# Kernel optimization log

Measured on AMD Instinct MI355X. Metric: run time of the kernel, lower is better.

## Reference

```python
import jax, jax.numpy as jnp
import numpy as np

N = 50000      # total nodes in batched graph
E = 800000     # total edges (avg degree 16)
B = 512        # number of graphs in batch
F_IN = 74      # input node feature size
H = 64         # hidden size per layer
OUT = 64       # output_feats
EPS = 1e-5     # BatchNorm eps


def setup_inputs() -> dict:
    key = jax.random.key(0)
    ks = jax.random.split(key, 32)
    d = {}
    d['feats'] = jax.random.normal(ks[0], (N, F_IN), dtype=jnp.float32)
    d['src'] = jax.random.randint(ks[1], (E,), 0, N)
    d['dst'] = jax.random.randint(ks[2], (E,), 0, N)
    d['graph_ids'] = jnp.sort(jax.random.randint(ks[3], (N,), 0, B))
    dims = [F_IN, H, H, H]
    i = 4
    for l in range(3):
        din, dout = dims[l], dims[l + 1]
        d[f'W{l}'] = jax.random.normal(ks[i], (din, dout), jnp.float32) / np.sqrt(din).astype(np.float32); i += 1
        d[f'b{l}'] = jnp.zeros((dout,), jnp.float32)
        d[f'rW{l}'] = jax.random.normal(ks[i], (din, dout), jnp.float32) / np.sqrt(din).astype(np.float32); i += 1
        d[f'rb{l}'] = jnp.zeros((dout,), jnp.float32)
        d[f'g{l}'] = jnp.ones((dout,), jnp.float32)    # BN gamma
        d[f'be{l}'] = jnp.zeros((dout,), jnp.float32)  # BN beta
    d['aw_W'] = jax.random.normal(ks[i], (H, 1), jnp.float32) / np.sqrt(H).astype(np.float32); i += 1
    d['aw_b'] = jnp.zeros((1,), jnp.float32)
    d['out_W'] = jax.random.normal(ks[i], (2 * H, OUT), jnp.float32) / np.sqrt(2 * H).astype(np.float32); i += 1
    d['out_b'] = jnp.zeros((OUT,), jnp.float32)
    return d


def _gcn_layer(x, src, dst, W, b, rW, rb, g, be):
    # GraphConv, norm='none': out = sum-aggregate(X W) + b, then relu
    xw = x @ W                                                    # [N, dout]
    agg = jax.ops.segment_sum(xw[src], dst, num_segments=N) + b   # gather/scatter over edges
    h = jax.nn.relu(agg)
    # residual: relu(Linear(x))
    h = h + jax.nn.relu(x @ rW + rb)
    # dropout p=0 -> identity
    # BatchNorm1d (training-mode batch statistics, biased variance)
    mean = jnp.mean(h, axis=0)
    var = jnp.var(h, axis=0)
    return (h - mean) * jax.lax.rsqrt(var + EPS) * g + be


def reference(feats, src, dst, graph_ids,
              W0, b0, rW0, rb0, g0, be0,
              W1, b1, rW1, rb1, g1, be1,
              W2, b2, rW2, rb2, g2, be2,
              aw_W, aw_b, out_W, out_b):
    h = feats
    h = _gcn_layer(h, src, dst, W0, b0, rW0, rb0, g0, be0)
    h = _gcn_layer(h, src, dst, W1, b1, rW1, rb1, g1, be1)
    h = _gcn_layer(h, src, dst, W2, b2, rW2, rb2, g2, be2)
    # WeightedSumAndMax readout
    w = jax.nn.sigmoid(h @ aw_W + aw_b)                               # [N, 1]
    h_sum = jax.ops.segment_sum(h * w, graph_ids, num_segments=B)     # [B, H]
    h_max = jax.ops.segment_max(h, graph_ids, num_segments=B)         # [B, H]
    h_max = jnp.where(jnp.isfinite(h_max), h_max, 0.0)                # empty graphs -> 0 (dgl max_nodes)
    h_g = jnp.concatenate([h_sum, h_max], axis=1)                     # [B, 2H]
    return h_g @ out_W + out_b                                        # [B, OUT]
```

## Files before the change

### kernel.cpp

```cpp
#include <hip/hip_runtime.h>
#include <hip/hip_bf16.h>
#include <math.h>

#define NN 50000
#define NE 800000
#define NB 512
#define FIN 74
#define HD 64
#define BN_EPS 1e-5f

#define CHUNK 32
#define ELLW 32
#define NBLK ((NN + CHUNK - 1) / CHUNK)
#define NBUCK2 NBLK
#define EB2 128
#define EPB (NE / EB2)
#define OCAPW 96


__global__ __launch_bounds__(256) void hist2_kernel(const int* __restrict__ dst,
                                                    int* __restrict__ H,
                                                    float* __restrict__ stats012,
                                                    unsigned long long* __restrict__ xw_zrow,
                                                    const float* __restrict__ W0,
                                                    const float* __restrict__ rW0,
                                                    float2* __restrict__ Wpk0) {
    __shared__ int lh[NBUCK2];
    int b = blockIdx.x, tid = threadIdx.x;
    for (int i = tid; i < NBUCK2; i += 256) lh[i] = 0;
    __syncthreads();
    int e0 = b * EPB;
    for (int i = tid; i < EPB; i += 256) atomicAdd(&lh[dst[e0 + i] >> 5], 1);
    if (b == 0) {
        for (int i = tid; i < 384; i += 256) stats012[i] = 0.f;
        if (tid < 16) xw_zrow[tid] = 0ull;
        for (int i = tid; i < FIN * HD; i += 256) Wpk0[i] = make_float2(W0[i], rW0[i]);
    }
    __syncthreads();
    for (int i = tid; i < NBUCK2; i += 256) H[b * NBUCK2 + i] = lh[i];
}

__global__ __launch_bounds__(128) void scanA2_kernel(int* __restrict__ H, int* __restrict__ T) {
    __shared__ int l[128];
    int k = blockIdx.x, tid = threadIdx.x;
    int v = H[tid * NBUCK2 + k];
    l[tid] = v;
    __syncthreads();
    for (int off = 1; off < 128; off <<= 1) {
        int t = (tid >= off) ? l[tid - off] : 0;
        __syncthreads();
        l[tid] += t;
        __syncthreads();
    }
    H[tid * NBUCK2 + k] = l[tid] - v;
    if (tid == 127) T[k] = l[127];
}

__global__ __launch_bounds__(256) void scanB2_kernel(const int* __restrict__ T,
                                                     int* __restrict__ bbase) {
    __shared__ int l[256];
    __shared__ int carry;
    int tid = threadIdx.x;
    if (tid == 0) carry = 0;
    __syncthreads();
    for (int c0 = 0; c0 < NBUCK2; c0 += 256) {
        int v = (c0 + tid < NBUCK2) ? T[c0 + tid] : 0;
        l[tid] = v;
        __syncthreads();
        for (int off = 1; off < 256; off <<= 1) {
            int t = (tid >= off) ? l[tid - off] : 0;
            __syncthreads();
            l[tid] += t;
            __syncthreads();
        }
        if (c0 + tid < NBUCK2) bbase[c0 + tid] = l[tid] - v + carry;
        __syncthreads();
        if (tid == 0) carry += l[255];
        __syncthreads();
    }
    if (tid == 0) bbase[NBUCK2] = carry;
}

__global__ __launch_bounds__(256) void scatter2_kernel(const int* __restrict__ src,
                                                       const int* __restrict__ dst,
                                                       const int* __restrict__ H,
                                                       const int* __restrict__ bbase,
                                                       unsigned* __restrict__ pairs) {
    __shared__ int cur[NBUCK2];
    int b = blockIdx.x, tid = threadIdx.x;
    for (int i = tid; i < NBUCK2; i += 256) cur[i] = H[b * NBUCK2 + i] + bbase[i];
    __syncthreads();
    int e0 = b * EPB;
    for (int i = tid; i < EPB; i += 256) {
        int d = dst[e0 + i];
        int s = src[e0 + i];
        int pos = atomicAdd(&cur[d >> 5], 1);
        pairs[pos] = (unsigned)s | ((unsigned)(d & 31) << 17);
    }
}


template <int K>
__global__ __launch_bounds__(256) void gemm_dual_kernel(
    const float* __restrict__ x, const float2* __restrict__ Wpk,
    const float* __restrict__ rb, __hip_bfloat16* __restrict__ xw,
    __hip_bfloat16* __restrict__ res, int n) {
    __shared__ float2 sW[K * HD];
    __shared__ float srb[64];
    for (int i = threadIdx.x; i < K * HD; i += 256) sW[i] = Wpk[i];
    if (threadIdx.x < 64) srb[threadIdx.x] = rb[threadIdx.x];
    __syncthreads();
    int wl = threadIdx.x >> 6, lane = threadIdx.x & 63;
    for (int r0 = (blockIdx.x * 4 + wl) * 8; r0 < n; r0 += gridDim.x * 32) {
        float a1[8], a2[8];
#pragma unroll
        for (int r = 0; r < 8; ++r) { a1[r] = 0.f; a2[r] = 0.f; }
#pragma unroll
        for (int c0 = 0; c0 < K; c0 += 64) {
            const int cl = (K - c0 < 64) ? (K - c0) : 64;
            float xv[8];
#pragma unroll
            for (int r = 0; r < 8; ++r) {
                int row = r0 + r;
                xv[r] = (lane < cl && row < n) ? x[(size_t)row * K + c0 + lane] : 0.f;
            }
#pragma unroll 16
            for (int j = 0; j < cl; ++j) {
                float2 w = sW[(c0 + j) * HD + lane];
#pragma unroll
                for (int r = 0; r < 8; ++r) {
                    float xb = __uint_as_float(
                        __builtin_amdgcn_readlane(__float_as_uint(xv[r]), j));
                    a1[r] = fmaf(xb, w.x, a1[r]);
                    a2[r] = fmaf(xb, w.y, a2[r]);
                }
            }
        }
#pragma unroll
        for (int r = 0; r < 8; ++r) {
            int row = r0 + r;
            if (row < n) {
                xw[(size_t)row * HD + lane] = __float2bfloat16(a1[r]);
                res[(size_t)row * HD + lane] = __float2bfloat16(fmaxf(a2[r] + srb[lane], 0.f));
            }
        }
    }
}

__global__ void fold_kernel(const float* __restrict__ stats, const float* __restrict__ g,
                            const float* __restrict__ be, const float* __restrict__ W,
                            const float* __restrict__ rW, const float* __restrict__ rb,
                            float2* __restrict__ Wpk, float* __restrict__ shiftW,
                            float* __restrict__ rbp) {
    __shared__ float sc[64], sh[64];
    int t = threadIdx.x;
    if (t < 64) {
        float mean = stats[t] / (float)NN;
        float var = stats[64 + t] / (float)NN - mean * mean;
        float scale = g[t] * rsqrtf(var + BN_EPS);
        sc[t] = scale;
        sh[t] = be[t] - mean * scale;
    }
    __syncthreads();
    for (int i = t; i < 64 * 64; i += 256) {
        int k = i >> 6;
        Wpk[i] = make_float2(sc[k] * W[i], sc[k] * rW[i]);
    }
    if (t < 64) {
        float sw = 0.f, srw = 0.f;
        for (int k = 0; k < 64; ++k) {
            sw = fmaf(sh[k], W[k * 64 + t], sw);
            srw = fmaf(sh[k], rW[k * 64 + t], srw);
        }
        shiftW[t] = sw;
        rbp[t] = rb[t] + srw;
    }
}

__device__ __forceinline__ float bf_lo(unsigned int p) { return __uint_as_float(p << 16); }
__device__ __forceinline__ float bf_hi(unsigned int p) { return __uint_as_float(p & 0xffff0000u); }

#define GATHER16(BASE)                                             \
    {                                                              \
        unsigned long long d[16];                                  \
        _Pragma("unroll") for (int j = 0; j < 16; ++j) {           \
            int idx = myIdx[(BASE) + j];                           \
            unsigned off = (unsigned)idx * 16u + (unsigned)c8;     \
            d[j] = XWu[off];                                       \
        }                                                          \
        _Pragma("unroll") for (int j = 0; j < 16; ++j) {           \
            unsigned lo = (unsigned)d[j], hi = (unsigned)(d[j] >> 32); \
            a0 += bf_lo(lo); a1 += bf_hi(lo);                      \
            a2 += bf_lo(hi); a3 += bf_hi(hi);                      \
        }                                                          \
    }

__global__ __launch_bounds__(256, 6) void fused_agg_kernel(
    const __hip_bfloat16* __restrict__ xw, const __hip_bfloat16* __restrict__ res,
    const float* __restrict__ b, const float* __restrict__ shiftW,
    const int* __restrict__ bbase, const unsigned* __restrict__ pairs,
    float* __restrict__ hout, float* __restrict__ stats, int n) {
    __shared__ int sIdx[4][8][ELLW + 1];
    __shared__ int sLen[4][8];
    __shared__ unsigned oflow[4][OCAPW];
    __shared__ int ocnt[4];
    __shared__ float lsr[4][16][8];

    int tid = threadIdx.x;
    int wl = tid >> 6, lane = tid & 63;
    int r0 = blockIdx.x * CHUNK;

    for (int i = lane; i < 8 * (ELLW + 1); i += 64) ((int*)sIdx[wl])[i] = NN;
    if (lane < 8) sLen[wl][lane] = 0;
    if (lane == 0) ocnt[wl] = 0;

    int beg = bbase[blockIdx.x], end = bbase[blockIdx.x + 1];
    for (int i = beg + lane; i < end; i += 64) {
        unsigned v = pairs[i];
        int rloc = (int)(v >> 17);
        if ((rloc >> 3) == wl) {
            int r8 = rloc & 7;
            int rk = atomicAdd(&sLen[wl][r8], 1);
            if (rk < ELLW) {
                sIdx[wl][r8][rk] = (int)(v & 0x1FFFFu);
            } else {
                int o = atomicAdd(&ocnt[wl], 1);
                if (o < OCAPW) oflow[wl][o] = v;
            }
        }
    }
    int nof = ocnt[wl];
    int noflow = (nof < OCAPW) ? nof : OCAPW;

    const unsigned long long* XWu = (const unsigned long long*)xw;
    const unsigned long long* REu = (const unsigned long long*)res;
    int q = lane >> 4, c8 = lane & 15;
    float4 bv = *(const float4*)&b[4 * c8];
    float4 swv = shiftW ? *(const float4*)&shiftW[4 * c8] : make_float4(0.f, 0.f, 0.f, 0.f);
    float s0 = 0.f, s1 = 0.f, s2 = 0.f, s3 = 0.f;
    float q0 = 0.f, q1 = 0.f, q2 = 0.f, q3 = 0.f;

#pragma unroll
    for (int p = 0; p < 2; ++p) {
        int r8 = p * 4 + q;
        int grow = r0 + wl * 8 + r8;
        int growc = (grow < n) ? grow : (n - 1);
        int l0 = sLen[wl][p * 4], l1 = sLen[wl][p * 4 + 1];
        int l2 = sLen[wl][p * 4 + 2], l3 = sLen[wl][p * 4 + 3];
        int m01 = (l0 > l1) ? l0 : l1, m23 = (l2 > l3) ? l2 : l3;
        int kmax = (m01 > m23) ? m01 : m23;
        int mylen = sLen[wl][r8];
        const int* myIdx = sIdx[wl][r8];
        unsigned long long rqw = REu[(unsigned)growc * 16u + (unsigned)c8];
        float a0 = 0.f, a1 = 0.f, a2 = 0.f, a3 = 0.f;
        GATHER16(0)
        if (kmax > 16) GATHER16(16)
        if (kmax > ELLW) {
            int myrloc = wl * 8 + r8;
            for (int o = 0; o < noflow; ++o) {
                unsigned v = oflow[wl][o];
                if ((int)(v >> 17) == myrloc) {
                    unsigned off = (v & 0x1FFFFu) * 16u + (unsigned)c8;
                    unsigned long long u = XWu[off];
                    unsigned lo = (unsigned)u, hi = (unsigned)(u >> 32);
                    a0 += bf_lo(lo); a1 += bf_hi(lo);
                    a2 += bf_lo(hi); a3 += bf_hi(hi);
                }
            }
        }
        unsigned rlo = (unsigned)rqw, rhi = (unsigned)(rqw >> 32);
        float dg = (float)mylen;
        float h0 = fmaxf(a0 + fmaf(dg, swv.x, bv.x), 0.f) + bf_lo(rlo);
        float h1 = fmaxf(a1 + fmaf(dg, swv.y, bv.y), 0.f) + bf_hi(rlo);
        float h2 = fmaxf(a2 + fmaf(dg, swv.z, bv.z), 0.f) + bf_lo(rhi);
        float h3 = fmaxf(a3 + fmaf(dg, swv.w, bv.w), 0.f) + bf_hi(rhi);
        if (grow < n) {
            *(float4*)&hout[(unsigned)grow * 64u + 4u * c8] = make_float4(h0, h1, h2, h3);
            s0 += h0; s1 += h1; s2 += h2; s3 += h3;
            q0 += h0 * h0; q1 += h1 * h1; q2 += h2 * h2; q3 += h3 * h3;
        }
    }

    s0 += __shfl_xor(s0, 16, 64); s0 += __shfl_xor(s0, 32, 64);
    s1 += __shfl_xor(s1, 16, 64); s1 += __shfl_xor(s1, 32, 64);
    s2 += __shfl_xor(s2, 16, 64); s2 += __shfl_xor(s2, 32, 64);
    s3 += __shfl_xor(s3, 16, 64); s3 += __shfl_xor(s3, 32, 64);
    q0 += __shfl_xor(q0, 16, 64); q0 += __shfl_xor(q0, 32, 64);
    q1 += __shfl_xor(q1, 16, 64); q1 += __shfl_xor(q1, 32, 64);
    q2 += __shfl_xor(q2, 16, 64); q2 += __shfl_xor(q2, 32, 64);
    q3 += __shfl_xor(q3, 16, 64); q3 += __shfl_xor(q3, 32, 64);
    if (q == 0) {
        lsr[wl][c8][0] = s0; lsr[wl][c8][1] = s1; lsr[wl][c8][2] = s2; lsr[wl][c8][3] = s3;
        lsr[wl][c8][4] = q0; lsr[wl][c8][5] = q1; lsr[wl][c8][6] = q2; lsr[wl][c8][7] = q3;
    }
    __syncthreads();
    if (tid < 64) {
        int c8i = tid >> 2, comp = tid & 3;
        float ssum = lsr[0][c8i][comp] + lsr[1][c8i][comp] + lsr[2][c8i][comp] + lsr[3][c8i][comp];
        float qsum = lsr[0][c8i][4 + comp] + lsr[1][c8i][4 + comp] + lsr[2][c8i][4 + comp] +
                     lsr[3][c8i][4 + comp];
        atomicAdd(&stats[tid], ssum);
        atomicAdd(&stats[64 + tid], qsum);
    }
}


__global__ void readout_init_kernel(float* __restrict__ hsum, unsigned int* __restrict__ hmax,
                                    const float* __restrict__ stats, const float* __restrict__ g,
                                    const float* __restrict__ be, float* __restrict__ ss) {
    int idx = blockIdx.x * 256 + threadIdx.x;
    if (idx < NB * HD) {
        hsum[idx] = 0.f;
        hmax[idx] = 0x007FFFFFu;
    }
    if (blockIdx.x == 0 && threadIdx.x < 64) {
        int c = threadIdx.x;
        float mean = stats[c] / (float)NN;
        float var = stats[64 + c] / (float)NN - mean * mean;
        float scale = g[c] * rsqrtf(var + BN_EPS);
        ss[c] = scale;
        ss[64 + c] = be[c] - mean * scale;
    }
}

#define RNODES 16

__device__ __forceinline__ void ro_flush(float* hsum, unsigned int* hmax, int g, int c,
                                         float accS, float accM) {
    atomicAdd(&hsum[g * HD + c], accS);
    unsigned int bits = __float_as_uint(accM);
    unsigned int enc = (bits & 0x80000000u) ? ~bits : (bits | 0x80000000u);
    atomicMax(&hmax[g * HD + c], enc);
}

__global__ __launch_bounds__(256) void readout_kernel(
    const float* __restrict__ h, const int* __restrict__ gid, const float* __restrict__ ss,
    const float* __restrict__ awW, const float* __restrict__ awb, float* __restrict__ hsum,
    unsigned int* __restrict__ hmax, int n) {
    int wid = blockIdx.x * 4 + (threadIdx.x >> 6);
    int c = threadIdx.x & 63;
    int r0 = wid * RNODES;
    if (r0 >= n) return;
    int r1 = r0 + RNODES;
    if (r1 > n) r1 = n;
    float aw = awW[c], ab = awb[0];
    float sA = ss[c], sB = ss[64 + c];
    int cur = gid[r0];
    float accS = 0.f, accM = -__builtin_inff();
    for (int r = r0; r < r1; ++r) {
        int g = gid[r];
        if (g != cur) {
            ro_flush(hsum, hmax, cur, c, accS, accM);
            accS = 0.f;
            accM = -__builtin_inff();
            cur = g;
        }
        float v = fmaf(h[(size_t)r * HD + c], sA, sB);
        float p = v * aw;
        for (int off = 32; off; off >>= 1) p += __shfl_xor(p, off, 64);
        float w = 1.f / (1.f + expf(-(p + ab)));
        accS = fmaf(v, w, accS);
        accM = fmaxf(accM, v);
    }
    ro_flush(hsum, hmax, cur, c, accS, accM);
}

__global__ void final_kernel(const float* __restrict__ hsum, const unsigned int* __restrict__ hmax,
                             const float* __restrict__ outW, const float* __restrict__ outb,
                             float* __restrict__ out) {
    __shared__ float sW[128 * 64];
    for (int i = threadIdx.x; i < 128 * 64; i += 256) sW[i] = outW[i];
    __syncthreads();
    int idx = blockIdx.x * 256 + threadIdx.x;
    if (idx >= NB * HD) return;
    int bi = idx >> 6, o = idx & 63;
    float acc = outb[o];
#pragma unroll 4
    for (int k = 0; k < 64; ++k) acc = fmaf(hsum[bi * 64 + k], sW[k * 64 + o], acc);
#pragma unroll 4
    for (int k = 0; k < 64; ++k) {
        unsigned int e = hmax[bi * 64 + k];
        float m;
        if (e == 0x007FFFFFu) {
            m = 0.f;
        } else {
            m = (e & 0x80000000u) ? __uint_as_float(e ^ 0x80000000u) : __uint_as_float(~e);
        }
        acc = fmaf(m, sW[(64 + k) * 64 + o], acc);
    }
    out[idx] = acc;
}


extern "C" void kernel_launch(void* const* d_in, const int* in_sizes, int n_in,
                              void* d_out, int out_size, void* d_ws, size_t ws_size,
                              hipStream_t stream) {
    const float* feats = (const float*)d_in[0];
    const int* src = (const int*)d_in[1];
    const int* dst = (const int*)d_in[2];
    const int* gid = (const int*)d_in[3];
    const float* W[3];
    const float* b[3];
    const float* rW[3];
    const float* rb[3];
    const float* g[3];
    const float* be[3];
    for (int l = 0; l < 3; ++l) {
        W[l] = (const float*)d_in[4 + 6 * l + 0];
        b[l] = (const float*)d_in[4 + 6 * l + 1];
        rW[l] = (const float*)d_in[4 + 6 * l + 2];
        rb[l] = (const float*)d_in[4 + 6 * l + 3];
        g[l] = (const float*)d_in[4 + 6 * l + 4];
        be[l] = (const float*)d_in[4 + 6 * l + 5];
    }
    const float* awW = (const float*)d_in[22];
    const float* awb = (const float*)d_in[23];
    const float* outW = (const float*)d_in[24];
    const float* outb = (const float*)d_in[25];
    float* out = (float*)d_out;

    __hip_bfloat16* XW = (__hip_bfloat16*)d_ws;
    __hip_bfloat16* RES = XW + (size_t)(NN + 1) * HD;
    float* P1 = (float*)(RES + (size_t)NN * HD);
    float* stats = P1 + (size_t)NN * HD;
    float* ss2 = stats + 384;
    float2* WPK = (float2*)(ss2 + 128);
    float* shW = (float*)(WPK + FIN * HD);
    float* rbp = shW + 64;
    float* hsum = rbp + 64;
    unsigned int* hmax = (unsigned int*)(hsum + (size_t)NB * HD);
    unsigned* pairs = (unsigned*)(hmax + (size_t)NB * HD);
    int* H = (int*)(pairs + (size_t)NE);
    int* T = H + (size_t)EB2 * NBUCK2;
    int* bbase = T + NBUCK2;

    float* stats0 = stats;
    float* stats1 = stats + 128;
    float* stats2 = stats + 256;

    const int GEMMBLK = 1280;
    const int ROBLK = (NN + RNODES * 4 - 1) / (RNODES * 4);

    hist2_kernel<<<EB2, 256, 0, stream>>>(dst, H, stats,
                                          (unsigned long long*)(XW + (size_t)NN * HD),
                                          W[0], rW[0], WPK);
    scanA2_kernel<<<NBUCK2, 128, 0, stream>>>(H, T);
    scanB2_kernel<<<1, 256, 0, stream>>>(T, bbase);
    scatter2_kernel<<<EB2, 256, 0, stream>>>(src, dst, H, bbase, pairs);

    gemm_dual_kernel<FIN><<<GEMMBLK, 256, 0, stream>>>(feats, WPK, rb[0], XW, RES, NN);
    fused_agg_kernel<<<NBLK, 256, 0, stream>>>(XW, RES, b[0], (const float*)nullptr, bbase,
                                               pairs, P1, stats0, NN);

    fold_kernel<<<1, 256, 0, stream>>>(stats0, g[0], be[0], W[1], rW[1], rb[1], WPK, shW, rbp);
    gemm_dual_kernel<HD><<<GEMMBLK, 256, 0, stream>>>(P1, WPK, rbp, XW, RES, NN);
    fused_agg_kernel<<<NBLK, 256, 0, stream>>>(XW, RES, b[1], shW, bbase, pairs, P1, stats1, NN);

    fold_kernel<<<1, 256, 0, stream>>>(stats1, g[1], be[1], W[2], rW[2], rb[2], WPK, shW, rbp);
    gemm_dual_kernel<HD><<<GEMMBLK, 256, 0, stream>>>(P1, WPK, rbp, XW, RES, NN);
    fused_agg_kernel<<<NBLK, 256, 0, stream>>>(XW, RES, b[2], shW, bbase, pairs, P1, stats2, NN);

    readout_init_kernel<<<(NB * HD + 255) / 256, 256, 0, stream>>>(hsum, hmax, stats2, g[2], be[2], ss2);
    readout_kernel<<<ROBLK, 256, 0, stream>>>(P1, gid, ss2, awW, awb, hsum, hmax, NN);
    final_kernel<<<(NB * HD + 255) / 256, 256, 0, stream>>>(hsum, hmax, outW, outb, out);
}
```

Before: 322.2 us.

## Store packed GEMM weights as bf16 pairs and retune edge-bucket and GEMM grids

Packs the folded W and rW weights into one 32-bit word holding two bf16 values instead of a float2. This halves the shared-memory footprint and LDS traffic in the dual GEMM, at the cost of lower weight precision. It also doubles the number of edge-histogram blocks, with the scan block size following EB2, and lowers the GEMM grid from 1280 to 782 blocks. The smaller shared-memory allocation may let more GEMM blocks stay resident per CU. The bf16 weights add rounding error before each BatchNorm stage.

```diff
diff --git a/kernel.cpp b/kernel.cpp
--- a/kernel.cpp
+++ b/kernel.cpp
@@ -13,9 +13,15 @@
 #define ELLW 32
 #define NBLK ((NN + CHUNK - 1) / CHUNK)
 #define NBUCK2 NBLK
-#define EB2 128
+#define EB2 256
 #define EPB (NE / EB2)
 #define OCAPW 96
+
+__device__ __forceinline__ unsigned pack_bf2(float a, float b) {
+    __hip_bfloat16 ha = __float2bfloat16(a), hb = __float2bfloat16(b);
+    unsigned short ua = *(unsigned short*)&ha, ub = *(unsigned short*)&hb;
+    return (unsigned)ua | ((unsigned)ub << 16);
+}
 
 
 __global__ __launch_bounds__(256) void hist2_kernel(const int* __restrict__ dst,
@@ -24,7 +30,7 @@
                                                     unsigned long long* __restrict__ xw_zrow,
                                                     const float* __restrict__ W0,
                                                     const float* __restrict__ rW0,
-                                                    float2* __restrict__ Wpk0) {
+                                                    unsigned* __restrict__ Wpk0) {
     __shared__ int lh[NBUCK2];
     int b = blockIdx.x, tid = threadIdx.x;
     for (int i = tid; i < NBUCK2; i += 256) lh[i] = 0;
@@ -34,26 +40,26 @@
     if (b == 0) {
         for (int i = tid; i < 384; i += 256) stats012[i] = 0.f;
         if (tid < 16) xw_zrow[tid] = 0ull;
-        for (int i = tid; i < FIN * HD; i += 256) Wpk0[i] = make_float2(W0[i], rW0[i]);
+        for (int i = tid; i < FIN * HD; i += 256) Wpk0[i] = pack_bf2(W0[i], rW0[i]);
     }
     __syncthreads();
     for (int i = tid; i < NBUCK2; i += 256) H[b * NBUCK2 + i] = lh[i];
 }
 
-__global__ __launch_bounds__(128) void scanA2_kernel(int* __restrict__ H, int* __restrict__ T) {
-    __shared__ int l[128];
+__global__ __launch_bounds__(EB2) void scanA2_kernel(int* __restrict__ H, int* __restrict__ T) {
+    __shared__ int l[EB2];
     int k = blockIdx.x, tid = threadIdx.x;
     int v = H[tid * NBUCK2 + k];
     l[tid] = v;
     __syncthreads();
-    for (int off = 1; off < 128; off <<= 1) {
+    for (int off = 1; off < EB2; off <<= 1) {
         int t = (tid >= off) ? l[tid - off] : 0;
         __syncthreads();
         l[tid] += t;
         __syncthreads();
     }
     H[tid * NBUCK2 + k] = l[tid] - v;
-    if (tid == 127) T[k] = l[127];
+    if (tid == EB2 - 1) T[k] = l[EB2 - 1];
 }
 
 __global__ __launch_bounds__(256) void scanB2_kernel(const int* __restrict__ T,
@@ -102,10 +108,10 @@
 
 template <int K>
 __global__ __launch_bounds__(256) void gemm_dual_kernel(
-    const float* __restrict__ x, const float2* __restrict__ Wpk,
+    const float* __restrict__ x, const unsigned* __restrict__ Wpk,
     const float* __restrict__ rb, __hip_bfloat16* __restrict__ xw,
     __hip_bfloat16* __restrict__ res, int n) {
-    __shared__ float2 sW[K * HD];
+    __shared__ unsigned sW[K * HD];
     __shared__ float srb[64];
     for (int i = threadIdx.x; i < K * HD; i += 256) sW[i] = Wpk[i];
     if (threadIdx.x < 64) srb[threadIdx.x] = rb[threadIdx.x];
@@ -126,13 +132,15 @@
             }
 #pragma unroll 16
             for (int j = 0; j < cl; ++j) {
-                float2 w = sW[(c0 + j) * HD + lane];
+                unsigned w = sW[(c0 + j) * HD + lane];
+                float w1 = __uint_as_float(w << 16);
+                float w2 = __uint_as_float(w & 0xffff0000u);
 #pragma unroll
                 for (int r = 0; r < 8; ++r) {
                     float xb = __uint_as_float(
                         __builtin_amdgcn_readlane(__float_as_uint(xv[r]), j));
-                    a1[r] = fmaf(xb, w.x, a1[r]);
-                    a2[r] = fmaf(xb, w.y, a2[r]);
+                    a1[r] = fmaf(xb, w1, a1[r]);
+                    a2[r] = fmaf(xb, w2, a2[r]);
                 }
             }
         }
@@ -150,7 +158,7 @@
 __global__ void fold_kernel(const float* __restrict__ stats, const float* __restrict__ g,
                             const float* __restrict__ be, const float* __restrict__ W,
                             const float* __restrict__ rW, const float* __restrict__ rb,
-                            float2* __restrict__ Wpk, float* __restrict__ shiftW,
+                            unsigned* __restrict__ Wpk, float* __restrict__ shiftW,
                             float* __restrict__ rbp) {
     __shared__ float sc[64], sh[64];
     int t = threadIdx.x;
@@ -164,7 +172,7 @@
     __syncthreads();
     for (int i = t; i < 64 * 64; i += 256) {
         int k = i >> 6;
-        Wpk[i] = make_float2(sc[k] * W[i], sc[k] * rW[i]);
+        Wpk[i] = pack_bf2(sc[k] * W[i], sc[k] * rW[i]);
     }
     if (t < 64) {
         float sw = 0.f, srw = 0.f;
@@ -424,7 +432,7 @@
     float* P1 = (float*)(RES + (size_t)NN * HD);
     float* stats = P1 + (size_t)NN * HD;
     float* ss2 = stats + 384;
-    float2* WPK = (float2*)(ss2 + 128);
+    unsigned* WPK = (unsigned*)(ss2 + 128);
     float* shW = (float*)(WPK + FIN * HD);
     float* rbp = shW + 64;
     float* hsum = rbp + 64;
@@ -438,13 +446,13 @@
     float* stats1 = stats + 128;
     float* stats2 = stats + 256;
 
-    const int GEMMBLK = 1280;
+    const int GEMMBLK = 782;
     const int ROBLK = (NN + RNODES * 4 - 1) / (RNODES * 4);
 
     hist2_kernel<<<EB2, 256, 0, stream>>>(dst, H, stats,
                                           (unsigned long long*)(XW + (size_t)NN * HD),
                                           W[0], rW[0], WPK);
-    scanA2_kernel<<<NBUCK2, 128, 0, stream>>>(H, T);
+    scanA2_kernel<<<NBUCK2, EB2, 0, stream>>>(H, T);
     scanB2_kernel<<<1, 256, 0, stream>>>(T, bbase);
     scatter2_kernel<<<EB2, 256, 0, stream>>>(src, dst, H, bbase, pairs);
 
```

Result: slower. 334.6 us (+3.9%).
